# Kernel tuning notes

Measured on AMD Instinct MI355X. Metric: run time of the kernel, lower is better.

Reference implementation:

```python
import jax, jax.numpy as jnp
import numpy as np

NUM_EXPERTS = 8
TOP_K = 2
HIDDEN = 1024
INTER = 1408


def setup_inputs() -> dict:
    key = jax.random.key(0)
    k0, k1, k2, k3, k4 = jax.random.split(key, 5)
    B, S = 2, 2048
    d_scale = HIDDEN ** -0.5
    i_scale = INTER ** -0.5
    return {
        "hidden_states": jax.random.normal(k0, (B, S, HIDDEN), jnp.float32),
        # nn.Linear(hidden, num_experts, bias=False): weight (E, d)
        "gate_w": jax.random.normal(k1, (NUM_EXPERTS, HIDDEN), jnp.float32) * d_scale,
        # per-expert SwiGLU weights, nn.Linear convention (out, in)
        "gate_proj": jax.random.normal(k2, (NUM_EXPERTS, INTER, HIDDEN), jnp.float32) * d_scale,
        "up_proj": jax.random.normal(k3, (NUM_EXPERTS, INTER, HIDDEN), jnp.float32) * d_scale,
        "down_proj": jax.random.normal(k4, (NUM_EXPERTS, HIDDEN, INTER), jnp.float32) * i_scale,
    }


def reference(hidden_states, gate_w, gate_proj, up_proj, down_proj):
    B, S, D = hidden_states.shape
    x = hidden_states.reshape(-1, D)  # (T, d)
    T = x.shape[0]

    # gate linear -> router logits (T, E)
    router_logits = x @ gate_w.T

    # TopKRouter: softmax in fp32 over all experts, top-k, optional renorm
    probs = jax.nn.softmax(router_logits.astype(jnp.float32), axis=-1)
    routing_weights, selected_experts = jax.lax.top_k(probs, TOP_K)  # (T, k)
    routing_weights = routing_weights / routing_weights.sum(axis=-1, keepdims=True)  # norm_topk_prob
    routing_weights = routing_weights.astype(x.dtype)

    # combine weights per (token, expert): scatter top-k weights into dense (T, E)
    combine = jnp.zeros((T, NUM_EXPERTS), x.dtype).at[
        jnp.arange(T)[:, None], selected_experts
    ].add(routing_weights)

    # per-expert SwiGLU FFN, weighted combine (loop over small fixed expert set)
    out = jnp.zeros_like(x)
    for e in range(NUM_EXPERTS):
        h = jax.nn.silu(x @ gate_proj[e].T) * (x @ up_proj[e].T)  # (T, i)
        out = out + combine[:, e : e + 1] * (h @ down_proj[e].T)  # (T, d)

    return out.reshape(B, S, D), router_logits
```

## Files before the change

### kernel.cpp

```cpp
#include <hip/hip_runtime.h>
#include <hip/hip_bf16.h>
#include <stdint.h>

#define T_TOK 4096
#define DH 1024
#define DI 1408
#define NE 8
#define TOPK 2
#define PADROWS 9216

typedef short s16x8 __attribute__((ext_vector_type(8)));
typedef float f32x4 __attribute__((ext_vector_type(4)));

__device__ inline unsigned f2bf(float f) {
    __hip_bfloat16 h = __float2bfloat16(f);
    return (unsigned)*(unsigned short*)&h;
}
__device__ inline float bf2f(unsigned short u) {
    return __uint_as_float(((unsigned)u) << 16);
}

#define GLDS(src, dst) __builtin_amdgcn_global_load_lds( \
    (const __attribute__((address_space(1))) void*)(src), \
    (__attribute__((address_space(3))) void*)(dst), 16, 0, 0)

__global__ __launch_bounds__(256) void cvt3_kernel(const float* __restrict__ s0,
        const float* __restrict__ s1, const float* __restrict__ s2,
        uint4* __restrict__ t0, uint4* __restrict__ t1, uint4* __restrict__ t2, int n8) {
    int i = blockIdx.x * blockDim.x + threadIdx.x;
    int stride = gridDim.x * blockDim.x;
    const float4* f0 = (const float4*)s0;
    const float4* f1 = (const float4*)s1;
    const float4* f2 = (const float4*)s2;
    for (; i < n8; i += stride) {
        float4 a0 = f0[2 * i], b0 = f0[2 * i + 1];
        float4 a1 = f1[2 * i], b1 = f1[2 * i + 1];
        float4 a2 = f2[2 * i], b2 = f2[2 * i + 1];
        uint4 o0, o1, o2;
        o0.x = f2bf(a0.x) | (f2bf(a0.y) << 16); o0.y = f2bf(a0.z) | (f2bf(a0.w) << 16);
        o0.z = f2bf(b0.x) | (f2bf(b0.y) << 16); o0.w = f2bf(b0.z) | (f2bf(b0.w) << 16);
        o1.x = f2bf(a1.x) | (f2bf(a1.y) << 16); o1.y = f2bf(a1.z) | (f2bf(a1.w) << 16);
        o1.z = f2bf(b1.x) | (f2bf(b1.y) << 16); o1.w = f2bf(b1.z) | (f2bf(b1.w) << 16);
        o2.x = f2bf(a2.x) | (f2bf(a2.y) << 16); o2.y = f2bf(a2.z) | (f2bf(a2.w) << 16);
        o2.z = f2bf(b2.x) | (f2bf(b2.y) << 16); o2.w = f2bf(b2.z) | (f2bf(b2.w) << 16);
        t0[i] = o0; t1[i] = o1; t2[i] = o2;
    }
}

__global__ __launch_bounds__(256) void router_kernel(const float* __restrict__ x,
                              const float* __restrict__ gw,
                              float* __restrict__ logits_out,
                              int* __restrict__ tokE, float* __restrict__ tokW,
                              unsigned short* __restrict__ xb) {
    int wave = threadIdx.x >> 6;
    int lane = threadIdx.x & 63;
    int t = blockIdx.x * 4 + wave;
    const float4* xr = (const float4*)(x + (size_t)t * DH);

    float acc[NE];
#pragma unroll
    for (int e = 0; e < NE; ++e) acc[e] = 0.f;

#pragma unroll
    for (int i = 0; i < 4; ++i) {
        float4 xv = xr[lane + i * 64];
#pragma unroll
        for (int e = 0; e < NE; ++e) {
            float4 g = ((const float4*)(gw + (size_t)e * DH))[lane + i * 64];
            acc[e] += xv.x * g.x + xv.y * g.y + xv.z * g.z + xv.w * g.w;
        }
        uint2 o;
        o.x = f2bf(xv.x) | (f2bf(xv.y) << 16);
        o.y = f2bf(xv.z) | (f2bf(xv.w) << 16);
        *(uint2*)(xb + (size_t)t * DH + (lane + i * 64) * 4) = o;
    }
#pragma unroll
    for (int e = 0; e < NE; ++e) {
#pragma unroll
        for (int off = 32; off > 0; off >>= 1) acc[e] += __shfl_xor(acc[e], off, 64);
    }
    if (lane == 0) {
        float mx = acc[0];
#pragma unroll
        for (int e = 1; e < NE; ++e) mx = fmaxf(mx, acc[e]);
        float p[NE]; float s = 0.f;
#pragma unroll
        for (int e = 0; e < NE; ++e) { p[e] = expf(acc[e] - mx); s += p[e]; }
        float inv = 1.f / s;
#pragma unroll
        for (int e = 0; e < NE; ++e) p[e] *= inv;
        int i0 = 0, i1 = -1; float p0 = -1.f, p1 = -1.f;
#pragma unroll
        for (int e = 0; e < NE; ++e) {
            float v = p[e];
            if (v > p0) { p1 = p0; i1 = i0; p0 = v; i0 = e; }
            else if (v > p1) { p1 = v; i1 = e; }
        }
        float wsum = p0 + p1;
#pragma unroll
        for (int e = 0; e < NE; ++e) logits_out[(size_t)t * NE + e] = acc[e];
        tokE[2 * t]     = i0;  tokE[2 * t + 1] = i1;
        tokW[2 * t]     = p0 / wsum;  tokW[2 * t + 1] = p1 / wsum;
    }
}

__global__ __launch_bounds__(1024) void histscatter_kernel(const int* __restrict__ tokE,
        int* __restrict__ countsG, int* __restrict__ padOffG,
        int* __restrict__ assignTok, int* __restrict__ tokSlot) {
    __shared__ int wc[16][NE];
    __shared__ int padOff[NE + 1];
    __shared__ int cursor[NE];
    int tid = threadIdx.x, wave = tid >> 6, lane = tid & 63;

    int cnt[NE];
#pragma unroll
    for (int e = 0; e < NE; ++e) cnt[e] = 0;
    for (int i = tid; i < T_TOK * TOPK; i += 1024) {
        int v = tokE[i];
#pragma unroll
        for (int e = 0; e < NE; ++e)
            cnt[e] += (int)__popcll(__ballot(v == e));
    }
    if (lane == 0) {
#pragma unroll
        for (int e = 0; e < NE; ++e) wc[wave][e] = cnt[e];
    }
    __syncthreads();
    if (tid == 0) {
        int r = 0;
        for (int e = 0; e < NE; ++e) {
            int c = 0;
            for (int w = 0; w < 16; ++w) c += wc[w][e];
            countsG[e] = c;
            padOff[e] = r;
            padOffG[e] = r;
            cursor[e] = 0;
            r += ((c + 127) >> 7) << 7;
        }
        padOff[NE] = r;
        padOffG[NE] = r;
    }
    __syncthreads();

    unsigned long long lmask = (1ull << lane) - 1ull;
    for (int i = tid; i < T_TOK * TOPK; i += 1024) {
        int e = tokE[i];
#pragma unroll
        for (int ex = 0; ex < NE; ++ex) {
            unsigned long long m = __ballot(e == ex);
            if (e == ex) {
                int rank = (int)__popcll(m & lmask);
                int leader = __ffsll((long long)m) - 1;
                int b = 0;
                if (rank == 0) b = atomicAdd(&cursor[ex], (int)__popcll(m));
                b = __shfl(b, leader, 64);
                int slot = padOff[ex] + b + rank;
                assignTok[slot] = i >> 1;
                tokSlot[i] = slot;
            }
        }
    }
}

__global__ __launch_bounds__(512) void gemmA_kernel(
        const unsigned short* __restrict__ xb,
        const unsigned short* __restrict__ gpb, const unsigned short* __restrict__ upb,
        const int* __restrict__ padOff, const int* __restrict__ assignTok,
        unsigned short* __restrict__ h) {
    int bid = blockIdx.x;
    int nid = (bid & 7) * 99 + (bid >> 3);
    int colblk = nid / 72, rowblk = nid - colblk * 72;
    int pr0 = rowblk * 128;
    int n0 = colblk * 128;
    int e = -1;
#pragma unroll
    for (int i = 0; i < NE; ++i)
        if (pr0 >= padOff[i] && pr0 < padOff[i + 1]) e = i;
    if (e < 0) return;

    __shared__ unsigned short As[2][128 * 32];
    __shared__ unsigned short Bgs[2][128 * 32];
    __shared__ unsigned short Bus[2][128 * 32];

    int tid = threadIdx.x;
    int lane = tid & 63;
    int w = tid >> 6;
    int wm = (w >> 2) * 64;
    int wn = (w & 3) * 32;

    int srow = w * 16 + (lane >> 2);
    int aslot = (((lane & 3) ^ ((lane >> 3) & 3)) << 3);
    int tok = assignTok[pr0 + srow];
    const unsigned short* a0   = xb  + (size_t)tok * DH + aslot;
    const unsigned short* gsrc = gpb + ((size_t)e * DI + n0 + srow) * DH + aslot;
    const unsigned short* usrc = upb + ((size_t)e * DI + n0 + srow) * DH + aslot;
    int sdst = w * 512;

    int rq = (((lane >> 4) ^ ((lane >> 1) & 3)) << 3);

    f32x4 accG[4][2], accU[4][2];
#pragma unroll
    for (int i = 0; i < 4; ++i)
#pragma unroll
        for (int j = 0; j < 2; ++j) {
            accG[i][j] = (f32x4){0.f, 0.f, 0.f, 0.f};
            accU[i][j] = (f32x4){0.f, 0.f, 0.f, 0.f};
        }

#define STAGE_A(buf, k0) do { \
    GLDS(a0 + (k0),   &As[buf][sdst]); \
    GLDS(gsrc + (k0), &Bgs[buf][sdst]); \
    GLDS(usrc + (k0), &Bus[buf][sdst]); \
    } while (0)

#define KCOMP_A(cur, VMS) do { \
    asm volatile("s_waitcnt vmcnt(" VMS ")" ::: "memory"); \
    __builtin_amdgcn_s_barrier(); \
    __builtin_amdgcn_sched_barrier(0); \
    s16x8 af[4], bgf[2], bu2[2]; \
    _Pragma("unroll") \
    for (int i = 0; i < 4; ++i) \
        af[i] = *(const s16x8*)&As[cur][(wm + 16 * i + (lane & 15)) * 32 + rq]; \
    _Pragma("unroll") \
    for (int j = 0; j < 2; ++j) { \
        bgf[j] = *(const s16x8*)&Bgs[cur][(wn + 16 * j + (lane & 15)) * 32 + rq]; \
        bu2[j] = *(const s16x8*)&Bus[cur][(wn + 16 * j + (lane & 15)) * 32 + rq]; \
    } \
    asm volatile("s_waitcnt lgkmcnt(0)" ::: "memory"); \
    __builtin_amdgcn_sched_barrier(0); \
    __builtin_amdgcn_s_barrier(); \
    __builtin_amdgcn_sched_barrier(0); \
    _Pragma("unroll") \
    for (int i = 0; i < 4; ++i) \
        _Pragma("unroll") \
        for (int j = 0; j < 2; ++j) { \
            accG[i][j] = __builtin_amdgcn_mfma_f32_16x16x32_bf16(af[i], bgf[j], accG[i][j], 0, 0, 0); \
            accU[i][j] = __builtin_amdgcn_mfma_f32_16x16x32_bf16(af[i], bu2[j], accU[i][j], 0, 0, 0); \
        } \
    } while (0)

    STAGE_A(0, 0);
    for (int ks = 0; ks < 31; ++ks) {
        STAGE_A((ks + 1) & 1, (ks + 1) * 32);
        KCOMP_A(ks & 1, "3");
    }
    KCOMP_A(1, "0");
#undef STAGE_A
#undef KCOMP_A

#pragma unroll
    for (int i = 0; i < 4; ++i) {
        int rowb = pr0 + wm + 16 * i + ((lane >> 4) << 2);
#pragma unroll
        for (int j = 0; j < 2; ++j) {
            int col = n0 + wn + 16 * j + (lane & 15);
#pragma unroll
            for (int r = 0; r < 4; ++r) {
                float g = accG[i][j][r], u = accU[i][j][r];
                float val = (g / (1.f + __expf(-g))) * u;
                h[(size_t)(rowb + r) * DI + col] = (unsigned short)f2bf(val);
            }
        }
    }
}

__global__ __launch_bounds__(256) void gemmB_kernel(
        const unsigned short* __restrict__ h,
        const unsigned short* __restrict__ dpb,
        const int* __restrict__ padOff, const int* __restrict__ counts,
        unsigned short* __restrict__ outP) {
    int bid = blockIdx.x;
    int nid = (bid & 7) * 72 + (bid >> 3);
    int colblk = nid / 72, rowblk = nid - colblk * 72;
    int pr0 = rowblk * 128;
    int n0 = colblk * 128;
    int e = -1, base = 0;
#pragma unroll
    for (int i = 0; i < NE; ++i)
        if (pr0 >= padOff[i] && pr0 < padOff[i + 1]) { e = i; base = padOff[i]; }
    if (e < 0) return;
    int cnt = counts[e];

    __shared__ unsigned short As[2][128 * 32];
    __shared__ unsigned short Bs[2][128 * 32];

    int tid = threadIdx.x;
    int lane = tid & 63;
    int w = tid >> 6;
    int wm = (w >> 1) * 64;
    int wn = (w & 1) * 64;

    int srow = w * 32 + (lane >> 2);
    int aslot = (((lane & 3) ^ ((lane >> 3) & 3)) << 3);
    const unsigned short* a0   = h   + (size_t)(pr0 + srow) * DI + aslot;
    const unsigned short* a1   = h   + (size_t)(pr0 + srow + 16) * DI + aslot;
    const unsigned short* b0   = dpb + ((size_t)e * DH + n0 + srow) * DI + aslot;
    const unsigned short* b1   = dpb + ((size_t)e * DH + n0 + srow + 16) * DI + aslot;
    int sdst = w * 1024;

    int rq = (((lane >> 4) ^ ((lane >> 1) & 3)) << 3);

    f32x4 acc[4][4];
#pragma unroll
    for (int i = 0; i < 4; ++i)
#pragma unroll
        for (int j = 0; j < 4; ++j) acc[i][j] = (f32x4){0.f, 0.f, 0.f, 0.f};

#define STAGE_B(buf, k0) do { \
    GLDS(a0 + (k0), &As[buf][sdst]); \
    GLDS(a1 + (k0), &As[buf][sdst + 512]); \
    GLDS(b0 + (k0), &Bs[buf][sdst]); \
    GLDS(b1 + (k0), &Bs[buf][sdst + 512]); \
    } while (0)

#define KCOMP_B(cur, VMS) do { \
    asm volatile("s_waitcnt vmcnt(" VMS ")" ::: "memory"); \
    __builtin_amdgcn_s_barrier(); \
    __builtin_amdgcn_sched_barrier(0); \
    s16x8 af[4], bf[4]; \
    _Pragma("unroll") \
    for (int i = 0; i < 4; ++i) \
        af[i] = *(const s16x8*)&As[cur][(wm + 16 * i + (lane & 15)) * 32 + rq]; \
    _Pragma("unroll") \
    for (int j = 0; j < 4; ++j) \
        bf[j] = *(const s16x8*)&Bs[cur][(wn + 16 * j + (lane & 15)) * 32 + rq]; \
    asm volatile("s_waitcnt lgkmcnt(0)" ::: "memory"); \
    __builtin_amdgcn_sched_barrier(0); \
    __builtin_amdgcn_s_barrier(); \
    __builtin_amdgcn_sched_barrier(0); \
    _Pragma("unroll") \
    for (int i = 0; i < 4; ++i) \
        _Pragma("unroll") \
        for (int j = 0; j < 4; ++j) \
            acc[i][j] = __builtin_amdgcn_mfma_f32_16x16x32_bf16(af[i], bf[j], acc[i][j], 0, 0, 0); \
    } while (0)

    STAGE_B(0, 0);
    for (int ks = 0; ks < 43; ++ks) {
        STAGE_B((ks + 1) & 1, (ks + 1) * 32);
        KCOMP_B(ks & 1, "4");
    }
    KCOMP_B(1, "0");
#undef STAGE_B
#undef KCOMP_B

#pragma unroll
    for (int i = 0; i < 4; ++i) {
        int rowb = pr0 + wm + 16 * i + ((lane >> 4) << 2);
#pragma unroll
        for (int r = 0; r < 4; ++r) {
            int prow = rowb + r;
            if (prow - base < cnt) {
#pragma unroll
                for (int j = 0; j < 4; ++j) {
                    int col = n0 + wn + 16 * j + (lane & 15);
                    outP[(size_t)prow * DH + col] = (unsigned short)f2bf(acc[i][j][r]);
                }
            }
        }
    }
}

__global__ __launch_bounds__(256) void combine_kernel(const unsigned short* __restrict__ outP,
        const int* __restrict__ tokSlot, const float* __restrict__ tokW,
        float* __restrict__ out) {
    int t = blockIdx.x;
    int c = threadIdx.x * 4;
    int s0 = tokSlot[2 * t], s1 = tokSlot[2 * t + 1];
    float w0 = tokW[2 * t], w1 = tokW[2 * t + 1];
    ushort4 a = *(const ushort4*)(outP + (size_t)s0 * DH + c);
    ushort4 b = *(const ushort4*)(outP + (size_t)s1 * DH + c);
    float4 o;
    o.x = w0 * bf2f(a.x) + w1 * bf2f(b.x);
    o.y = w0 * bf2f(a.y) + w1 * bf2f(b.y);
    o.z = w0 * bf2f(a.z) + w1 * bf2f(b.z);
    o.w = w0 * bf2f(a.w) + w1 * bf2f(b.w);
    *(float4*)(out + (size_t)t * DH + c) = o;
}

extern "C" void kernel_launch(void* const* d_in, const int* in_sizes, int n_in,
                              void* d_out, int out_size, void* d_ws, size_t ws_size,
                              hipStream_t stream) {
    const float* x  = (const float*)d_in[0];
    const float* gw = (const float*)d_in[1];
    const float* gp = (const float*)d_in[2];
    const float* up = (const float*)d_in[3];
    const float* dp = (const float*)d_in[4];
    float* out = (float*)d_out;
    float* logits = out + (size_t)T_TOK * DH;

    char* ws = (char*)d_ws;
    int*   counts    = (int*)(ws + 0);
    int*   padOff    = (int*)(ws + 128);
    int*   tokE      = (int*)(ws + 4096);
    float* tokW      = (float*)(ws + 36864);
    int*   tokSlot   = (int*)(ws + 69632);
    int*   assignTok = (int*)(ws + 102400);
    unsigned short* xb   = (unsigned short*)(ws + 147456);
    unsigned short* gpb  = (unsigned short*)(ws + 8536064);
    unsigned short* upb  = (unsigned short*)(ws + 31604736);
    unsigned short* dpb  = (unsigned short*)(ws + 54673408);
    unsigned short* h    = (unsigned short*)(ws + 77742080);
    unsigned short* outP = (unsigned short*)(ws + 8536064);

    hipMemsetAsync(ws + 102400, 0, PADROWS * 4, stream);

    const int NW8 = NE * DI * DH / 8;
    cvt3_kernel<<<2048, 256, 0, stream>>>(gp, up, dp, (uint4*)gpb, (uint4*)upb, (uint4*)dpb, NW8);

    router_kernel<<<T_TOK / 4, 256, 0, stream>>>(x, gw, logits, tokE, tokW, xb);
    histscatter_kernel<<<1, 1024, 0, stream>>>(tokE, counts, padOff, assignTok, tokSlot);

    gemmA_kernel<<<dim3((DI / 128) * (PADROWS / 128)), 512, 0, stream>>>(xb, gpb, upb, padOff, assignTok, h);
    gemmB_kernel<<<dim3((DH / 128) * (PADROWS / 128)), 256, 0, stream>>>(h, dpb, padOff, counts, outP);
    combine_kernel<<<T_TOK, 256, 0, stream>>>(outP, tokSlot, tokW, out);
}
```

Measured before the change: 188.4 us.

## Triple-buffer GEMM LDS stages and fold assignTok zeroing into histscatter

Both expert GEMM kernels move from double to triple LDS buffering, keeping two k-stages of global-to-LDS loads in flight with adjusted vmcnt waits. The separate memset of the assignment table is replaced by zeroing inside the histogram kernel, which removes one launch. The cost is more LDS per block (72 KB for gemmA), which may lower occupancy.

New measurement: 185.1 us, median of 2. No clear change (-1.7%).

```diff
diff --git a/kernel.cpp b/kernel.cpp
--- a/kernel.cpp
+++ b/kernel.cpp
@@ -23,6 +23,9 @@
 #define GLDS(src, dst) __builtin_amdgcn_global_load_lds( \
     (const __attribute__((address_space(1))) void*)(src), \
     (__attribute__((address_space(3))) void*)(dst), 16, 0, 0)
+
+#define SBAR()  __builtin_amdgcn_s_barrier()
+#define SCHED() __builtin_amdgcn_sched_barrier(0)
 
 __global__ __launch_bounds__(256) void cvt3_kernel(const float* __restrict__ s0,
         const float* __restrict__ s1, const float* __restrict__ s2,
@@ -121,6 +124,7 @@
         for (int e = 0; e < NE; ++e)
             cnt[e] += (int)__popcll(__ballot(v == e));
     }
+    for (int i = tid; i < PADROWS; i += 1024) assignTok[i] = 0;
     if (lane == 0) {
 #pragma unroll
         for (int e = 0; e < NE; ++e) wc[wave][e] = cnt[e];
@@ -178,9 +182,9 @@
         if (pr0 >= padOff[i] && pr0 < padOff[i + 1]) e = i;
     if (e < 0) return;
 
-    __shared__ unsigned short As[2][128 * 32];
-    __shared__ unsigned short Bgs[2][128 * 32];
-    __shared__ unsigned short Bus[2][128 * 32];
+    __shared__ unsigned short As[3][128 * 32];
+    __shared__ unsigned short Bgs[3][128 * 32];
+    __shared__ unsigned short Bus[3][128 * 32];
 
     int tid = threadIdx.x;
     int lane = tid & 63;
@@ -215,8 +219,7 @@
 
 #define KCOMP_A(cur, VMS) do { \
     asm volatile("s_waitcnt vmcnt(" VMS ")" ::: "memory"); \
-    __builtin_amdgcn_s_barrier(); \
-    __builtin_amdgcn_sched_barrier(0); \
+    SBAR(); SCHED(); \
     s16x8 af[4], bgf[2], bu2[2]; \
     _Pragma("unroll") \
     for (int i = 0; i < 4; ++i) \
@@ -227,9 +230,9 @@
         bu2[j] = *(const s16x8*)&Bus[cur][(wn + 16 * j + (lane & 15)) * 32 + rq]; \
     } \
     asm volatile("s_waitcnt lgkmcnt(0)" ::: "memory"); \
-    __builtin_amdgcn_sched_barrier(0); \
-    __builtin_amdgcn_s_barrier(); \
-    __builtin_amdgcn_sched_barrier(0); \
+    SCHED(); \
+    SBAR(); \
+    SCHED(); \
     _Pragma("unroll") \
     for (int i = 0; i < 4; ++i) \
         _Pragma("unroll") \
@@ -240,10 +243,15 @@
     } while (0)
 
     STAGE_A(0, 0);
-    for (int ks = 0; ks < 31; ++ks) {
-        STAGE_A((ks + 1) & 1, (ks + 1) * 32);
-        KCOMP_A(ks & 1, "3");
-    }
+    STAGE_A(1, 32);
+    int bs = 2, bc = 0;
+    for (int ks = 0; ks < 30; ++ks) {
+        STAGE_A(bs, (ks + 2) * 32);
+        KCOMP_A(bc, "6");
+        bs = (bs == 2) ? 0 : bs + 1;
+        bc = (bc == 2) ? 0 : bc + 1;
+    }
+    KCOMP_A(0, "3");
     KCOMP_A(1, "0");
 #undef STAGE_A
 #undef KCOMP_A
@@ -281,8 +289,8 @@
     if (e < 0) return;
     int cnt = counts[e];
 
-    __shared__ unsigned short As[2][128 * 32];
-    __shared__ unsigned short Bs[2][128 * 32];
+    __shared__ unsigned short As[3][128 * 32];
+    __shared__ unsigned short Bs[3][128 * 32];
 
     int tid = threadIdx.x;
     int lane = tid & 63;
@@ -315,8 +323,7 @@
 
 #define KCOMP_B(cur, VMS) do { \
     asm volatile("s_waitcnt vmcnt(" VMS ")" ::: "memory"); \
-    __builtin_amdgcn_s_barrier(); \
-    __builtin_amdgcn_sched_barrier(0); \
+    SBAR(); SCHED(); \
     s16x8 af[4], bf[4]; \
     _Pragma("unroll") \
     for (int i = 0; i < 4; ++i) \
@@ -325,9 +332,9 @@
     for (int j = 0; j < 4; ++j) \
         bf[j] = *(const s16x8*)&Bs[cur][(wn + 16 * j + (lane & 15)) * 32 + rq]; \
     asm volatile("s_waitcnt lgkmcnt(0)" ::: "memory"); \
-    __builtin_amdgcn_sched_barrier(0); \
-    __builtin_amdgcn_s_barrier(); \
-    __builtin_amdgcn_sched_barrier(0); \
+    SCHED(); \
+    SBAR(); \
+    SCHED(); \
     _Pragma("unroll") \
     for (int i = 0; i < 4; ++i) \
         _Pragma("unroll") \
@@ -336,10 +343,15 @@
     } while (0)
 
     STAGE_B(0, 0);
-    for (int ks = 0; ks < 43; ++ks) {
-        STAGE_B((ks + 1) & 1, (ks + 1) * 32);
-        KCOMP_B(ks & 1, "4");
-    }
+    STAGE_B(1, 32);
+    int bs = 2, bc = 0;
+    for (int ks = 0; ks < 42; ++ks) {
+        STAGE_B(bs, (ks + 2) * 32);
+        KCOMP_B(bc, "8");
+        bs = (bs == 2) ? 0 : bs + 1;
+        bc = (bc == 2) ? 0 : bc + 1;
+    }
+    KCOMP_B(0, "4");
     KCOMP_B(1, "0");
 #undef STAGE_B
 #undef KCOMP_B
@@ -403,8 +415,6 @@
     unsigned short* h    = (unsigned short*)(ws + 77742080);
     unsigned short* outP = (unsigned short*)(ws + 8536064);
 
-    hipMemsetAsync(ws + 102400, 0, PADROWS * 4, stream);
-
     const int NW8 = NE * DI * DH / 8;
     cvt3_kernel<<<2048, 256, 0, stream>>>(gp, up, dp, (uint4*)gpb, (uint4*)upb, (uint4*)dpb, NW8);
 
@@ -412,6 +422,6 @@
     histscatter_kernel<<<1, 1024, 0, stream>>>(tokE, counts, padOff, assignTok, tokSlot);
 
     gemmA_kernel<<<dim3((DI / 128) * (PADROWS / 128)), 512, 0, stream>>>(xb, gpb, upb, padOff, assignTok, h);
-    gemmB_kernel<<<dim3((DH / 128) * (PADROWS / 128)), 256, 0, stream>>>(h, dpb, padOff, counts, outP);
+    gemmB_kernel<<<(DH / 128) * (PADROWS / 128), 256, 0, stream>>>(h, dpb, padOff, counts, outP);
     combine_kernel<<<T_TOK, 256, 0, stream>>>(outP, tokSlot, tokW, out);
 }
```
